# Optimization experiments

Hardware: AMD Instinct MI355X
Metric: run time of the kernel (lower is better)

## Reference

```python
import jax, jax.numpy as jnp
import numpy as np

LEAK_RATE = 0.5
SPECTRAL_RADIUS = 0.9
T, IN_DIM, R_DIM, OUT_DIM = 32768, 128, 1024, 64


def setup_inputs() -> dict:
    key = jax.random.key(0)
    k1, k2, k3, k4 = jax.random.split(key, 4)
    input_data = jax.random.normal(k1, (T, IN_DIM), dtype=jnp.float32)
    # reservoir weights with spectral radius normalization (as in __init__)
    W = np.array(jax.random.normal(k2, (R_DIM, R_DIM), dtype=jnp.float32), dtype=np.float64)
    W *= SPECTRAL_RADIUS / np.max(np.abs(np.linalg.eigvals(W)))
    reservoir_weights = jnp.asarray(W, dtype=jnp.float32)
    input_weights = jax.random.normal(k3, (R_DIM, IN_DIM), dtype=jnp.float32)
    output_weights = jax.random.normal(k4, (R_DIM, OUT_DIM), dtype=jnp.float32) * 0.02
    return {
        "input_data": input_data,
        "input_weights": input_weights,
        "reservoir_weights": reservoir_weights,
        "output_weights": output_weights,
    }


def reference(input_data, input_weights, reservoir_weights, output_weights):
    a = jnp.float32(LEAK_RATE)
    # precompute input projection for all timesteps: [T, R]
    u = input_data @ input_weights.T

    def step(s, u_t):
        s_dec = (1.0 - a) * s                      # decayed previous state
        s_new = s_dec + a * jnp.tanh(u_t + reservoir_weights @ s_dec)
        return s_new, s_new

    s0 = jnp.zeros((reservoir_weights.shape[0],), dtype=input_data.dtype)
    _, states = jax.lax.scan(step, s0, u)          # states: [T, R]
    predictions = states @ output_weights          # [T, OUT_DIM]
    return predictions
```

## Files before the change

### kernel.cpp

```cpp
#include <hip/hip_runtime.h>
#include <math.h>


#define G_BLOCKS 32
#define ROWS     32
#define TPB      256
#define T_STEPS  32768
#define R_DIM    1024
#define IN_DIM   128
#define OUT_DIM  64

__global__ __launch_bounds__(TPB, 1)
void esn_scan_kernel(const float* __restrict__ x,
                     const float* __restrict__ Win,
                     const float* __restrict__ W,
                     const float* __restrict__ Wout,
                     float* __restrict__ out,
                     unsigned long long* __restrict__ sbuf)
{
    constexpr float A   = 0.5f;
    constexpr float DEC = 0.5f;

    const int b    = blockIdx.x;
    const int tid  = threadIdx.x;
    const int lane = tid & 63;
    const int wave = tid >> 6;
    const int r    = tid & 31;
    const int kg   = tid >> 5;

    __shared__ float s_dec[R_DIM];
    __shared__ float part[8][ROWS];
    __shared__ float u_lds[2][ROWS];
    __shared__ float s_new_lds[ROWS];
    __shared__ float x_lds[2][IN_DIM];
    __shared__ float win_lds[ROWS * 132];
    __shared__ float wout_lds[ROWS * OUT_DIM];

    float w[128];
    {
        const float* wrow = W + ((size_t)(b * ROWS + r)) * R_DIM + kg * 128;
        #pragma unroll
        for (int j = 0; j < 128; j += 4) {
            const float4 v = *(const float4*)(wrow + j);
            w[j] = v.x; w[j+1] = v.y; w[j+2] = v.z; w[j+3] = v.w;
        }
    }
    for (int i = tid; i < ROWS * IN_DIM; i += TPB) {
        int rr = i >> 7, cc = i & 127;
        win_lds[rr * 132 + cc] = Win[((size_t)(b * ROWS + rr)) * IN_DIM + cc];
    }
    for (int i = tid; i < ROWS * OUT_DIM; i += TPB)
        wout_lds[i] = Wout[(size_t)b * ROWS * OUT_DIM + i];
    for (int i = tid; i < R_DIM; i += TPB) s_dec[i] = 0.0f;
    if (tid < IN_DIM) {
        x_lds[0][tid] = x[tid];
        x_lds[1][tid] = x[IN_DIM + tid];
    }
    __syncthreads();

    if (wave == 1) {
        int rr = lane & 31, kh = lane >> 5;
        float acc = 0.f;
        const float* wl = &win_lds[rr * 132 + kh * 64];
        const float* xl = &x_lds[0][kh * 64];
        #pragma unroll
        for (int i = 0; i < 64; i += 4) {
            float4 wv = *(const float4*)(wl + i);
            float4 xv = *(const float4*)(xl + i);
            acc += wv.x*xv.x + wv.y*xv.y + wv.z*xv.z + wv.w*xv.w;
        }
        acc += __shfl_down(acc, 32);
        if (lane < 32) u_lds[0][rr] = acc;
    }
    __syncthreads();

    for (int t = 0; t < T_STEPS; ++t) {
        {
            float a0 = 0.f, a1 = 0.f, a2 = 0.f, a3 = 0.f;
            const float* sp = &s_dec[kg * 128];
            #pragma unroll
            for (int j = 0; j < 128; j += 4) {
                const float4 sv = *(const float4*)(sp + j);
                a0 += w[j]   * sv.x;
                a1 += w[j+1] * sv.y;
                a2 += w[j+2] * sv.z;
                a3 += w[j+3] * sv.w;
            }
            part[kg][r] = (a0 + a1) + (a2 + a3);
        }
        __syncthreads();

        if (wave == 0) {
            float snew = 0.f;
            if (lane < 32) {
                float tot = 0.f;
                #pragma unroll
                for (int k = 0; k < 8; ++k) tot += part[k][lane];
                const float y  = u_lds[t & 1][lane] + tot;
                const float sd = s_dec[b * ROWS + lane];
                snew = sd + A * tanhf(y);
                s_new_lds[lane] = snew;
                const unsigned long long pkt =
                    ((unsigned long long)(unsigned int)(t + 1) << 32)
                    | (unsigned long long)__float_as_uint(snew);
                __hip_atomic_store(&sbuf[(size_t)(t & 1) * R_DIM + b * ROWS + lane],
                                   pkt, __ATOMIC_RELAXED, __HIP_MEMORY_SCOPE_AGENT);
            }
        } else if (wave == 1 && t + 1 < T_STEPS) {
            const int tpre = (t + 2 < T_STEPS) ? (t + 2) : (T_STEPS - 1);
            const float xv0 = x[(size_t)tpre * IN_DIM + lane];
            const float xv1 = x[(size_t)tpre * IN_DIM + 64 + lane];
            int rr = lane & 31, kh = lane >> 5;
            float acc = 0.f;
            const float* wl = &win_lds[rr * 132 + kh * 64];
            const float* xl = &x_lds[(t + 1) & 1][kh * 64];
            #pragma unroll
            for (int i = 0; i < 64; i += 4) {
                float4 wv = *(const float4*)(wl + i);
                float4 xv = *(const float4*)(xl + i);
                acc += wv.x*xv.x + wv.y*xv.y + wv.z*xv.z + wv.w*xv.w;
            }
            acc += __shfl_down(acc, 32);
            if (lane < 32) u_lds[(t + 1) & 1][rr] = acc;
            x_lds[t & 1][lane]      = xv0;
            x_lds[t & 1][64 + lane] = xv1;
        }
        __syncthreads();

        if (wave == 2) {
            float acc = 0.f;
            #pragma unroll
            for (int rr = 0; rr < 32; ++rr)
                acc += s_new_lds[rr] * wout_lds[rr * OUT_DIM + lane];
            atomicAdd(&out[(size_t)t * OUT_DIM + lane], acc);
        }
        if (t + 1 < T_STEPS) {
            const int want = t + 1;
            unsigned long long v[4];
            const size_t base = (size_t)(t & 1) * R_DIM;
            #pragma unroll
            for (int j = 0; j < 4; ++j)
                v[j] = __hip_atomic_load(&sbuf[base + j * TPB + tid],
                                         __ATOMIC_RELAXED, __HIP_MEMORY_SCOPE_AGENT);
            bool ok;
            do {
                ok = true;
                #pragma unroll
                for (int j = 0; j < 4; ++j) {
                    if ((int)(v[j] >> 32) != want) {
                        ok = false;
                        __builtin_amdgcn_s_sleep(1);
                        v[j] = __hip_atomic_load(&sbuf[base + j * TPB + tid],
                                                 __ATOMIC_RELAXED,
                                                 __HIP_MEMORY_SCOPE_AGENT);
                    }
                }
            } while (!ok);
            #pragma unroll
            for (int j = 0; j < 4; ++j)
                s_dec[j * TPB + tid] = __uint_as_float((unsigned int)v[j]) * DEC;
        }
        __syncthreads();
    }
}

extern "C" void kernel_launch(void* const* d_in, const int* in_sizes, int n_in,
                              void* d_out, int out_size, void* d_ws, size_t ws_size,
                              hipStream_t stream) {
    const float* x    = (const float*)d_in[0];
    const float* Win  = (const float*)d_in[1];
    const float* W    = (const float*)d_in[2];
    const float* Wout = (const float*)d_in[3];
    float* out = (float*)d_out;
    unsigned long long* sbuf = (unsigned long long*)d_ws;

    hipMemsetAsync(d_out, 0, (size_t)out_size * sizeof(float), stream);

    esn_scan_kernel<<<G_BLOCKS, TPB, 0, stream>>>(x, Win, W, Wout, out, sbuf);
}
```

Measured before the change: 69.05 ms.

## Double threads per block, round-robin full output projection across blocks, drop memset

Doubles the block to 512 threads so each thread holds 64 weights and the matvec runs with 16 partial groups. The per-block output projection with atomicAdd is replaced: each timestep one block, chosen round-robin, computes the full 1024x64 output row from the double-buffered decayed state. It reads Wout from global memory and writes the row directly, so the output memset goes away. One barrier per step is removed, and the spin-wait drops its sleep and polls each slot in a tight loop. The cost is more global traffic for the block doing the output row and more aggressive polling on the state buffer.

```diff
diff --git a/kernel.cpp b/kernel.cpp
--- a/kernel.cpp
+++ b/kernel.cpp
@@ -4,7 +4,7 @@
 
 #define G_BLOCKS 32
 #define ROWS     32
-#define TPB      256
+#define TPB      512
 #define T_STEPS  32768
 #define R_DIM    1024
 #define IN_DIM   128
@@ -18,8 +18,9 @@
                      float* __restrict__ out,
                      unsigned long long* __restrict__ sbuf)
 {
-    constexpr float A   = 0.5f;
-    constexpr float DEC = 0.5f;
+    constexpr float A       = 0.5f;
+    constexpr float DEC     = 0.5f;
+    constexpr float INV_DEC = 2.0f;
 
     const int b    = blockIdx.x;
     const int tid  = threadIdx.x;
@@ -28,19 +29,18 @@
     const int r    = tid & 31;
     const int kg   = tid >> 5;
 
-    __shared__ float s_dec[R_DIM];
-    __shared__ float part[8][ROWS];
+    __shared__ float s_dec[2][R_DIM];
+    __shared__ float part[16][ROWS];
+    __shared__ float part_out[16][OUT_DIM];
     __shared__ float u_lds[2][ROWS];
-    __shared__ float s_new_lds[ROWS];
     __shared__ float x_lds[2][IN_DIM];
     __shared__ float win_lds[ROWS * 132];
-    __shared__ float wout_lds[ROWS * OUT_DIM];
 
-    float w[128];
+    float w[64];
     {
-        const float* wrow = W + ((size_t)(b * ROWS + r)) * R_DIM + kg * 128;
+        const float* wrow = W + ((size_t)(b * ROWS + r)) * R_DIM + kg * 64;
         #pragma unroll
-        for (int j = 0; j < 128; j += 4) {
+        for (int j = 0; j < 64; j += 4) {
             const float4 v = *(const float4*)(wrow + j);
             w[j] = v.x; w[j+1] = v.y; w[j+2] = v.z; w[j+3] = v.w;
         }
@@ -49,9 +49,7 @@
         int rr = i >> 7, cc = i & 127;
         win_lds[rr * 132 + cc] = Win[((size_t)(b * ROWS + rr)) * IN_DIM + cc];
     }
-    for (int i = tid; i < ROWS * OUT_DIM; i += TPB)
-        wout_lds[i] = Wout[(size_t)b * ROWS * OUT_DIM + i];
-    for (int i = tid; i < R_DIM; i += TPB) s_dec[i] = 0.0f;
+    for (int i = tid; i < R_DIM; i += TPB) s_dec[0][i] = 0.0f;
     if (tid < IN_DIM) {
         x_lds[0][tid] = x[tid];
         x_lds[1][tid] = x[IN_DIM + tid];
@@ -74,12 +72,14 @@
     }
     __syncthreads();
 
-    for (int t = 0; t < T_STEPS; ++t) {
-        {
+    for (int t = 0; t <= T_STEPS + 1; ++t) {
+        const bool scan = (t < T_STEPS);
+
+        if (scan) {
             float a0 = 0.f, a1 = 0.f, a2 = 0.f, a3 = 0.f;
-            const float* sp = &s_dec[kg * 128];
+            const float* sp = &s_dec[t & 1][kg * 64];
             #pragma unroll
-            for (int j = 0; j < 128; j += 4) {
+            for (int j = 0; j < 64; j += 4) {
                 const float4 sv = *(const float4*)(sp + j);
                 a0 += w[j]   * sv.x;
                 a1 += w[j+1] * sv.y;
@@ -90,75 +90,81 @@
         }
         __syncthreads();
 
-        if (wave == 0) {
-            float snew = 0.f;
-            if (lane < 32) {
-                float tot = 0.f;
+        if (scan) {
+            if (wave == 0) {
+                if (lane < 32) {
+                    float tot = 0.f;
+                    #pragma unroll
+                    for (int k = 0; k < 16; ++k) tot += part[k][lane];
+                    const float y  = u_lds[t & 1][lane] + tot;
+                    const float sd = s_dec[t & 1][b * ROWS + lane];
+                    const float snew = sd + A * tanhf(y);
+                    const unsigned long long pkt =
+                        ((unsigned long long)(unsigned int)(t + 1) << 32)
+                        | (unsigned long long)__float_as_uint(snew);
+                    __hip_atomic_store(&sbuf[(size_t)(t & 1) * R_DIM + b * ROWS + lane],
+                                       pkt, __ATOMIC_RELAXED, __HIP_MEMORY_SCOPE_AGENT);
+                }
+            } else if (wave == 1 && t + 1 < T_STEPS) {
+                const int tpre = (t + 2 < T_STEPS) ? (t + 2) : (T_STEPS - 1);
+                const float xv0 = x[(size_t)tpre * IN_DIM + lane];
+                const float xv1 = x[(size_t)tpre * IN_DIM + 64 + lane];
+                int rr = lane & 31, kh = lane >> 5;
+                float acc = 0.f;
+                const float* wl = &win_lds[rr * 132 + kh * 64];
+                const float* xl = &x_lds[(t + 1) & 1][kh * 64];
                 #pragma unroll
-                for (int k = 0; k < 8; ++k) tot += part[k][lane];
-                const float y  = u_lds[t & 1][lane] + tot;
-                const float sd = s_dec[b * ROWS + lane];
-                snew = sd + A * tanhf(y);
-                s_new_lds[lane] = snew;
-                const unsigned long long pkt =
-                    ((unsigned long long)(unsigned int)(t + 1) << 32)
-                    | (unsigned long long)__float_as_uint(snew);
-                __hip_atomic_store(&sbuf[(size_t)(t & 1) * R_DIM + b * ROWS + lane],
-                                   pkt, __ATOMIC_RELAXED, __HIP_MEMORY_SCOPE_AGENT);
+                for (int i = 0; i < 64; i += 4) {
+                    float4 wv = *(const float4*)(wl + i);
+                    float4 xv = *(const float4*)(xl + i);
+                    acc += wv.x*xv.x + wv.y*xv.y + wv.z*xv.z + wv.w*xv.w;
+                }
+                acc += __shfl_down(acc, 32);
+                if (lane < 32) u_lds[(t + 1) & 1][rr] = acc;
+                x_lds[t & 1][lane]      = xv0;
+                x_lds[t & 1][64 + lane] = xv1;
             }
-        } else if (wave == 1 && t + 1 < T_STEPS) {
-            const int tpre = (t + 2 < T_STEPS) ? (t + 2) : (T_STEPS - 1);
-            const float xv0 = x[(size_t)tpre * IN_DIM + lane];
-            const float xv1 = x[(size_t)tpre * IN_DIM + 64 + lane];
-            int rr = lane & 31, kh = lane >> 5;
-            float acc = 0.f;
-            const float* wl = &win_lds[rr * 132 + kh * 64];
-            const float* xl = &x_lds[(t + 1) & 1][kh * 64];
-            #pragma unroll
-            for (int i = 0; i < 64; i += 4) {
-                float4 wv = *(const float4*)(wl + i);
-                float4 xv = *(const float4*)(xl + i);
-                acc += wv.x*xv.x + wv.y*xv.y + wv.z*xv.z + wv.w*xv.w;
+        }
+
+        if (wave >= 4 && t >= 1 && t <= T_STEPS && b == ((t - 1) & 31)) {
+            const int j  = tid - 256;
+            const int c4 = j & 15;
+            const int q  = j >> 4;
+            float4 acc = make_float4(0.f, 0.f, 0.f, 0.f);
+            const float* wo = Wout + (size_t)(q * 64) * OUT_DIM + c4 * 4;
+            const float* sv = &s_dec[t & 1][q * 64];
+            #pragma unroll 8
+            for (int rr = 0; rr < 64; ++rr) {
+                const float s = sv[rr];
+                const float4 wv = *(const float4*)(wo + (size_t)rr * OUT_DIM);
+                acc.x += s * wv.x; acc.y += s * wv.y;
+                acc.z += s * wv.z; acc.w += s * wv.w;
             }
-            acc += __shfl_down(acc, 32);
-            if (lane < 32) u_lds[(t + 1) & 1][rr] = acc;
-            x_lds[t & 1][lane]      = xv0;
-            x_lds[t & 1][64 + lane] = xv1;
+            *(float4*)&part_out[q][c4 * 4] = acc;
         }
-        __syncthreads();
 
-        if (wave == 2) {
+        if (wave == 4 && t >= 2 && b == ((t - 2) & 31)) {
             float acc = 0.f;
             #pragma unroll
-            for (int rr = 0; rr < 32; ++rr)
-                acc += s_new_lds[rr] * wout_lds[rr * OUT_DIM + lane];
-            atomicAdd(&out[(size_t)t * OUT_DIM + lane], acc);
+            for (int q = 0; q < 16; ++q) acc += part_out[q][lane];
+            out[(size_t)(t - 2) * OUT_DIM + lane] = acc * INV_DEC;
         }
-        if (t + 1 < T_STEPS) {
+
+        if (scan) {
             const int want = t + 1;
-            unsigned long long v[4];
             const size_t base = (size_t)(t & 1) * R_DIM;
-            #pragma unroll
-            for (int j = 0; j < 4; ++j)
-                v[j] = __hip_atomic_load(&sbuf[base + j * TPB + tid],
-                                         __ATOMIC_RELAXED, __HIP_MEMORY_SCOPE_AGENT);
-            bool ok;
-            do {
-                ok = true;
-                #pragma unroll
-                for (int j = 0; j < 4; ++j) {
-                    if ((int)(v[j] >> 32) != want) {
-                        ok = false;
-                        __builtin_amdgcn_s_sleep(1);
-                        v[j] = __hip_atomic_load(&sbuf[base + j * TPB + tid],
-                                                 __ATOMIC_RELAXED,
-                                                 __HIP_MEMORY_SCOPE_AGENT);
-                    }
-                }
-            } while (!ok);
-            #pragma unroll
-            for (int j = 0; j < 4; ++j)
-                s_dec[j * TPB + tid] = __uint_as_float((unsigned int)v[j]) * DEC;
+            unsigned long long v0 = __hip_atomic_load(&sbuf[base + tid],
+                                        __ATOMIC_RELAXED, __HIP_MEMORY_SCOPE_AGENT);
+            unsigned long long v1 = __hip_atomic_load(&sbuf[base + TPB + tid],
+                                        __ATOMIC_RELAXED, __HIP_MEMORY_SCOPE_AGENT);
+            while ((int)(v0 >> 32) != want)
+                v0 = __hip_atomic_load(&sbuf[base + tid],
+                                       __ATOMIC_RELAXED, __HIP_MEMORY_SCOPE_AGENT);
+            while ((int)(v1 >> 32) != want)
+                v1 = __hip_atomic_load(&sbuf[base + TPB + tid],
+                                       __ATOMIC_RELAXED, __HIP_MEMORY_SCOPE_AGENT);
+            s_dec[(t + 1) & 1][tid]       = __uint_as_float((unsigned int)v0) * DEC;
+            s_dec[(t + 1) & 1][TPB + tid] = __uint_as_float((unsigned int)v1) * DEC;
         }
         __syncthreads();
     }
@@ -174,7 +180,5 @@
     float* out = (float*)d_out;
     unsigned long long* sbuf = (unsigned long long*)d_ws;
 
-    hipMemsetAsync(d_out, 0, (size_t)out_size * sizeof(float), stream);
-
     esn_scan_kernel<<<G_BLOCKS, TPB, 0, stream>>>(x, Win, W, Wout, out, sbuf);
 }
```

Result: slower. 153.0 ms (+121.6%).
